# Optimization experiments

Measured on AMD Instinct MI355X. Metric: run time of the kernel, lower is better.

Reference implementation:

```python
import jax, jax.numpy as jnp
import numpy as np

B, L, D_MODEL, H, D_QKV = 4, 2048, 1024, 16, 64
SCALE = float(D_MODEL) ** 0.5  # note: source scales by sqrt(d_model), not sqrt(d_qkv)


def setup_inputs() -> dict:
    key = jax.random.key(0)
    ks = jax.random.split(key, 6)
    xavier_qkv = (2.0 / (D_MODEL + D_QKV)) ** 0.5
    xavier_fc = (2.0 / (H * D_QKV + D_MODEL)) ** 0.5
    return {
        "x": jax.random.normal(ks[0], (B, L, D_MODEL), dtype=jnp.float32),
        "mask": jnp.ones((B, L), dtype=jnp.int32),
        "w_q": jax.random.normal(ks[1], (H, D_MODEL, D_QKV), dtype=jnp.float32) * xavier_qkv,
        "w_k": jax.random.normal(ks[2], (H, D_MODEL, D_QKV), dtype=jnp.float32) * xavier_qkv,
        "w_v": jax.random.normal(ks[3], (H, D_MODEL, D_QKV), dtype=jnp.float32) * xavier_qkv,
        "fc_w": jax.random.normal(ks[4], (D_MODEL, H * D_QKV), dtype=jnp.float32) * xavier_fc,
        "fc_b": jnp.zeros((D_MODEL,), dtype=jnp.float32),
    }


def reference(x, mask, w_q, w_k, w_v, fc_w, fc_b):
    # x: [B, L, M]; per-head projections via einsum, as in the source
    q = jnp.einsum('blm,hmd->blhd', x, w_q)
    k = jnp.einsum('blm,hmd->blhd', x, w_k)
    v = jnp.einsum('blm,hmd->blhd', x, w_v)
    scores = jnp.einsum('blhd,bkhd->bhlk', q, k)  # [B, H, L, L]
    m = mask[:, None, None, :]  # unsqueeze(1).unsqueeze(2)
    scores = jnp.where(m == 0, jnp.asarray(-1e9, scores.dtype), scores)
    logits = jax.nn.softmax(scores / SCALE, axis=3)
    # Faithful to source einsum 'bhlk,blhd->blhd' (k is summed out of logits only)
    out = jnp.einsum('bhlk,blhd->blhd', logits, v)
    out = out.reshape(x.shape[0], x.shape[1], H * D_QKV)
    return out @ fc_w.T + fc_b
```

## Files before the change

### kernel.cpp

```cpp
#include <hip/hip_runtime.h>
#include <hip/hip_bf16.h>


typedef __attribute__((ext_vector_type(8))) short bf16x8;
typedef __attribute__((ext_vector_type(4))) float f32x4;
typedef __attribute__((ext_vector_type(4))) unsigned short u16x4;

__device__ __forceinline__ f32x4 mfma16(bf16x8 a, bf16x8 b, f32x4 c) {
  return __builtin_amdgcn_mfma_f32_16x16x32_bf16(a, b, c, 0, 0, 0);
}

__device__ __forceinline__ unsigned short f2b(float f) {
  unsigned int u = __builtin_bit_cast(unsigned int, f);
  return (unsigned short)((u + 0x7fffu + ((u >> 16) & 1u)) >> 16);
}

__device__ __forceinline__ bf16x8 cvt8(float4 a, float4 b) {
  bf16x8 r;
  r[0] = (short)f2b(a.x); r[1] = (short)f2b(a.y); r[2] = (short)f2b(a.z); r[3] = (short)f2b(a.w);
  r[4] = (short)f2b(b.x); r[5] = (short)f2b(b.y); r[6] = (short)f2b(b.z); r[7] = (short)f2b(b.w);
  return r;
}

__device__ __forceinline__ void gld_lds16(const void* g, void* l) {
  __builtin_amdgcn_global_load_lds((const __attribute__((address_space(1))) unsigned int*)g,
                                   (__attribute__((address_space(3))) unsigned int*)l, 16, 0, 0);
}

__global__ void cast4(const float* __restrict__ in, unsigned short* __restrict__ out) {
  int i = (blockIdx.x * 256 + threadIdx.x) * 4;
  float4 v = *reinterpret_cast<const float4*>(in + i);
  u16x4 o;
  o[0] = f2b(v.x); o[1] = f2b(v.y); o[2] = f2b(v.z); o[3] = f2b(v.w);
  *reinterpret_cast<u16x4*>(out + i) = o;
}

__global__ __launch_bounds__(256) void fold_w(const float* __restrict__ fcw,
                                              const float* __restrict__ wv,
                                              unsigned short* __restrict__ wcT) {
  int wid = threadIdx.x >> 6, lane = threadIdx.x & 63, l16 = lane & 15, quad = lane >> 4;
  int wr = wid >> 1, wc = wid & 1;
  int row0 = blockIdx.y * 64 + wr * 32;
  int col0 = blockIdx.x * 64 + wc * 32;
  f32x4 acc[2][2];
#pragma unroll
  for (int a = 0; a < 2; a++)
#pragma unroll
    for (int b = 0; b < 2; b++) acc[a][b] = (f32x4){0.f, 0.f, 0.f, 0.f};

  for (int k0 = 0; k0 < 1024; k0 += 32) {
    int kk = k0 + quad * 8;
    int h = kk >> 6, d = kk & 63;
    bf16x8 af[2], bfr[2];
#pragma unroll
    for (int rt = 0; rt < 2; rt++) {
      const float* pa = fcw + (row0 + rt * 16 + l16) * 1024 + kk;
      af[rt] = cvt8(*reinterpret_cast<const float4*>(pa), *reinterpret_cast<const float4*>(pa + 4));
    }
#pragma unroll
    for (int ct = 0; ct < 2; ct++) {
      const float* pb = wv + h * 65536 + (col0 + ct * 16 + l16) * 64 + d;
      bfr[ct] = cvt8(*reinterpret_cast<const float4*>(pb), *reinterpret_cast<const float4*>(pb + 4));
    }
#pragma unroll
    for (int rt = 0; rt < 2; rt++)
#pragma unroll
      for (int ct = 0; ct < 2; ct++) acc[rt][ct] = mfma16(af[rt], bfr[ct], acc[rt][ct]);
  }
#pragma unroll
  for (int rt = 0; rt < 2; rt++)
#pragma unroll
    for (int ct = 0; ct < 2; ct++) {
      int j0 = row0 + rt * 16 + quad * 4;
      int m = col0 + ct * 16 + l16;
#pragma unroll
      for (int r = 0; r < 4; r++) wcT[(j0 + r) * 1024 + m] = f2b(acc[rt][ct][r]);
    }
}

__global__ __launch_bounds__(256) void final_gemm(const unsigned short* __restrict__ xb,
                                                  const unsigned short* __restrict__ wcT,
                                                  const float* __restrict__ fcb,
                                                  float* __restrict__ out) {
  __shared__ __align__(16) unsigned short As[128 * 32];
  __shared__ __align__(16) unsigned short Bs[128 * 32];
  int t = threadIdx.x, wid = t >> 6, lane = t & 63, l16 = lane & 15, quad = lane >> 4;
  int wr = wid >> 1, wc = wid & 1;
  int row0 = blockIdx.x * 128;
  int col0 = blockIdx.y * 128;

  int sr = t >> 2, skq = t & 3;
  const unsigned short* Ag0 = xb + (row0 + sr) * 1024 + skq * 8;
  const unsigned short* Bg0 = wcT + (col0 + sr) * 1024 + skq * 8;

  f32x4 acc[16];
#pragma unroll
  for (int i = 0; i < 16; i++) acc[i] = (f32x4){0.f, 0.f, 0.f, 0.f};

  for (int k0 = 0; k0 < 1024; k0 += 32) {
    __syncthreads();
    gld_lds16(Ag0 + k0, &As[t * 8]);
    gld_lds16(Ag0 + 64 * 1024 + k0, &As[(256 + t) * 8]);
    gld_lds16(Bg0 + k0, &Bs[t * 8]);
    gld_lds16(Bg0 + 64 * 1024 + k0, &Bs[(256 + t) * 8]);
    __syncthreads();

    bf16x8 af[4], bfr[4];
#pragma unroll
    for (int rt = 0; rt < 4; rt++)
      af[rt] = *reinterpret_cast<const bf16x8*>(&As[(wr * 64 + rt * 16 + l16) * 32 + quad * 8]);
#pragma unroll
    for (int ct = 0; ct < 4; ct++)
      bfr[ct] = *reinterpret_cast<const bf16x8*>(&Bs[(wc * 64 + ct * 16 + l16) * 32 + quad * 8]);
#pragma unroll
    for (int rt = 0; rt < 4; rt++)
#pragma unroll
      for (int ct = 0; ct < 4; ct++)
        acc[rt * 4 + ct] = mfma16(af[rt], bfr[ct], acc[rt * 4 + ct]);
  }

#pragma unroll
  for (int ct = 0; ct < 4; ct++) {
    int j = col0 + wc * 64 + ct * 16 + l16;
    float bias = fcb[j];
#pragma unroll
    for (int rt = 0; rt < 4; rt++) {
      int i0 = row0 + wr * 64 + rt * 16 + quad * 4;
      f32x4 a = acc[rt * 4 + ct];
#pragma unroll
      for (int r = 0; r < 4; r++) out[(i0 + r) * 1024 + j] = a[r] + bias;
    }
  }
}

extern "C" void kernel_launch(void* const* d_in, const int* in_sizes, int n_in,
                              void* d_out, int out_size, void* d_ws, size_t ws_size,
                              hipStream_t stream) {
  const float* x   = (const float*)d_in[0];
  const float* wv  = (const float*)d_in[4];
  const float* fcw = (const float*)d_in[5];
  const float* fcb = (const float*)d_in[6];
  float* out = (float*)d_out;

  char* ws = (char*)d_ws;
  unsigned short* xb  = (unsigned short*)(ws);
  unsigned short* wcT = (unsigned short*)(ws + 16777216);

  cast4<<<8192, 256, 0, stream>>>(x, xb);
  fold_w<<<dim3(16, 16), 256, 0, stream>>>(fcw, wv, wcT);
  final_gemm<<<dim3(64, 8), 256, 0, stream>>>(xb, wcT, fcb, out);
}
```

Measured before the change: 153.5 us.

## Double K-step in final GEMM, split-K fold_w, and widen cast kernel

The final GEMM now stages 64 columns of K per barrier pair instead of 32, which halves the number of __syncthreads and load batches; each wave loads four 16-row blocks. fold_w runs 512 threads and splits K across two wave groups, combining their partial sums through shared memory, so the small 256-block grid has more parallelism. The cast kernel now converts 8 elements per thread with a 16-byte store. The price is more LDS per GEMM block, which may lower occupancy, and an extra shared-memory reduction in fold_w.

New measurement: 151.1 us. Within noise of the previous version (-1.6%).

```diff
diff --git a/kernel.cpp b/kernel.cpp
--- a/kernel.cpp
+++ b/kernel.cpp
@@ -4,7 +4,6 @@
 
 typedef __attribute__((ext_vector_type(8))) short bf16x8;
 typedef __attribute__((ext_vector_type(4))) float f32x4;
-typedef __attribute__((ext_vector_type(4))) unsigned short u16x4;
 
 __device__ __forceinline__ f32x4 mfma16(bf16x8 a, bf16x8 b, f32x4 c) {
   return __builtin_amdgcn_mfma_f32_16x16x32_bf16(a, b, c, 0, 0, 0);
@@ -27,19 +26,18 @@
                                    (__attribute__((address_space(3))) unsigned int*)l, 16, 0, 0);
 }
 
-__global__ void cast4(const float* __restrict__ in, unsigned short* __restrict__ out) {
-  int i = (blockIdx.x * 256 + threadIdx.x) * 4;
-  float4 v = *reinterpret_cast<const float4*>(in + i);
-  u16x4 o;
-  o[0] = f2b(v.x); o[1] = f2b(v.y); o[2] = f2b(v.z); o[3] = f2b(v.w);
-  *reinterpret_cast<u16x4*>(out + i) = o;
+__global__ void cast8(const float* __restrict__ in, unsigned short* __restrict__ out) {
+  int i = (blockIdx.x * 256 + threadIdx.x) * 8;
+  float4 a = *reinterpret_cast<const float4*>(in + i);
+  float4 b = *reinterpret_cast<const float4*>(in + i + 4);
+  *reinterpret_cast<bf16x8*>(out + i) = cvt8(a, b);
 }
 
-__global__ __launch_bounds__(256) void fold_w(const float* __restrict__ fcw,
+__global__ __launch_bounds__(512) void fold_w(const float* __restrict__ fcw,
                                               const float* __restrict__ wv,
                                               unsigned short* __restrict__ wcT) {
   int wid = threadIdx.x >> 6, lane = threadIdx.x & 63, l16 = lane & 15, quad = lane >> 4;
-  int wr = wid >> 1, wc = wid & 1;
+  int wk = wid >> 2, wr = (wid >> 1) & 1, wc = wid & 1;
   int row0 = blockIdx.y * 64 + wr * 32;
   int col0 = blockIdx.x * 64 + wc * 32;
   f32x4 acc[2][2];
@@ -48,7 +46,7 @@
 #pragma unroll
     for (int b = 0; b < 2; b++) acc[a][b] = (f32x4){0.f, 0.f, 0.f, 0.f};
 
-  for (int k0 = 0; k0 < 1024; k0 += 32) {
+  for (int k0 = wk * 512; k0 < wk * 512 + 512; k0 += 32) {
     int kk = k0 + quad * 8;
     int h = kk >> 6, d = kk & 63;
     bf16x8 af[2], bfr[2];
@@ -67,56 +65,82 @@
 #pragma unroll
       for (int ct = 0; ct < 2; ct++) acc[rt][ct] = mfma16(af[rt], bfr[ct], acc[rt][ct]);
   }
+
+  __shared__ f32x4 red[4][64][4];
+  if (wk == 1) {
 #pragma unroll
-  for (int rt = 0; rt < 2; rt++)
+    for (int rt = 0; rt < 2; rt++)
 #pragma unroll
-    for (int ct = 0; ct < 2; ct++) {
-      int j0 = row0 + rt * 16 + quad * 4;
-      int m = col0 + ct * 16 + l16;
+      for (int ct = 0; ct < 2; ct++) red[wid & 3][lane][rt * 2 + ct] = acc[rt][ct];
+  }
+  __syncthreads();
+  if (wk == 0) {
 #pragma unroll
-      for (int r = 0; r < 4; r++) wcT[(j0 + r) * 1024 + m] = f2b(acc[rt][ct][r]);
-    }
+    for (int rt = 0; rt < 2; rt++)
+#pragma unroll
+      for (int ct = 0; ct < 2; ct++) {
+        f32x4 s = acc[rt][ct];
+        f32x4 o = red[wid & 3][lane][rt * 2 + ct];
+        int j0 = row0 + rt * 16 + quad * 4;
+        int m = col0 + ct * 16 + l16;
+#pragma unroll
+        for (int r = 0; r < 4; r++) wcT[(j0 + r) * 1024 + m] = f2b(s[r] + o[r]);
+      }
+  }
 }
 
 __global__ __launch_bounds__(256) void final_gemm(const unsigned short* __restrict__ xb,
                                                   const unsigned short* __restrict__ wcT,
                                                   const float* __restrict__ fcb,
                                                   float* __restrict__ out) {
-  __shared__ __align__(16) unsigned short As[128 * 32];
-  __shared__ __align__(16) unsigned short Bs[128 * 32];
+  __shared__ __align__(16) unsigned short As[2 * 128 * 32];
+  __shared__ __align__(16) unsigned short Bs[2 * 128 * 32];
   int t = threadIdx.x, wid = t >> 6, lane = t & 63, l16 = lane & 15, quad = lane >> 4;
   int wr = wid >> 1, wc = wid & 1;
   int row0 = blockIdx.x * 128;
   int col0 = blockIdx.y * 128;
 
-  int sr = t >> 2, skq = t & 3;
-  const unsigned short* Ag0 = xb + (row0 + sr) * 1024 + skq * 8;
-  const unsigned short* Bg0 = wcT + (col0 + sr) * 1024 + skq * 8;
+  int w4 = wid * 4;
+  const unsigned short* Ap[4];
+  const unsigned short* Bp[4];
+#pragma unroll
+  for (int j = 0; j < 4; j++) {
+    int blk = w4 + j;
+    int s = blk >> 3, r0 = (blk & 7) * 16;
+    int row = r0 + (lane >> 2), kq = lane & 3;
+    Ap[j] = xb + (row0 + row) * 1024 + s * 32 + kq * 8;
+    Bp[j] = wcT + (col0 + row) * 1024 + s * 32 + kq * 8;
+  }
 
   f32x4 acc[16];
 #pragma unroll
   for (int i = 0; i < 16; i++) acc[i] = (f32x4){0.f, 0.f, 0.f, 0.f};
 
-  for (int k0 = 0; k0 < 1024; k0 += 32) {
+  for (int k0 = 0; k0 < 1024; k0 += 64) {
     __syncthreads();
-    gld_lds16(Ag0 + k0, &As[t * 8]);
-    gld_lds16(Ag0 + 64 * 1024 + k0, &As[(256 + t) * 8]);
-    gld_lds16(Bg0 + k0, &Bs[t * 8]);
-    gld_lds16(Bg0 + 64 * 1024 + k0, &Bs[(256 + t) * 8]);
+#pragma unroll
+    for (int j = 0; j < 4; j++) {
+      int off = (w4 + j) * 512 + lane * 8;
+      gld_lds16(Ap[j] + k0, &As[off]);
+      gld_lds16(Bp[j] + k0, &Bs[off]);
+    }
     __syncthreads();
 
-    bf16x8 af[4], bfr[4];
 #pragma unroll
-    for (int rt = 0; rt < 4; rt++)
-      af[rt] = *reinterpret_cast<const bf16x8*>(&As[(wr * 64 + rt * 16 + l16) * 32 + quad * 8]);
+    for (int s = 0; s < 2; s++) {
+      bf16x8 af[4], bfr[4];
 #pragma unroll
-    for (int ct = 0; ct < 4; ct++)
-      bfr[ct] = *reinterpret_cast<const bf16x8*>(&Bs[(wc * 64 + ct * 16 + l16) * 32 + quad * 8]);
-#pragma unroll
-    for (int rt = 0; rt < 4; rt++)
+      for (int rt = 0; rt < 4; rt++)
+        af[rt] = *reinterpret_cast<const bf16x8*>(&As[s * 4096 + (wr * 64 + rt * 16 + l16) * 32 + quad * 8]);
 #pragma unroll
       for (int ct = 0; ct < 4; ct++)
-        acc[rt * 4 + ct] = mfma16(af[rt], bfr[ct], acc[rt * 4 + ct]);
+        bfr[ct] = *reinterpret_cast<const bf16x8*>(&Bs[s * 4096 + (wc * 64 + ct * 16 + l16) * 32 + quad * 8]);
+#pragma unroll
+      for (int rt = 0; rt < 4; rt++)
+#pragma unroll
+        for (int ct = 0; ct < 4; ct++)
+          acc[rt * 4 + ct] = mfma16(af[rt], bfr[ct], acc[rt * 4 + ct]);
+    }
   }
 
 #pragma unroll
@@ -146,7 +170,7 @@
   unsigned short* xb  = (unsigned short*)(ws);
   unsigned short* wcT = (unsigned short*)(ws + 16777216);
 
-  cast4<<<8192, 256, 0, stream>>>(x, xb);
-  fold_w<<<dim3(16, 16), 256, 0, stream>>>(fcw, wv, wcT);
+  cast8<<<4096, 256, 0, stream>>>(x, xb);
+  fold_w<<<dim3(16, 16), 512, 0, stream>>>(fcw, wv, wcT);
   final_gemm<<<dim3(64, 8), 256, 0, stream>>>(xb, wcT, fcb, out);
 }
```
